# Kernel optimization log

Measured on AMD Instinct MI355X. Metric: run time of the kernel, lower is better.

Reference implementation:

```python
import jax, jax.numpy as jnp
import numpy as np

ALPHA = 1e-4
BETA = 1.0
MAX_STD = 1000.0
MIN_STD = 1.0
B = 8192            # number of ragged segments (batch)
NUM_CLASSES = 2
P = 1_000_000       # size of penalized parameter vector


def setup_inputs() -> dict:
    key = jax.random.key(0)
    k1, k2, k3, k4 = jax.random.split(key, 4)
    # ragged lengths: alternate 1024 / 3072, exact total T = B * 2048
    lengths = np.where(np.arange(B) % 2 == 0, 1024, 3072).astype(np.int32)
    T = int(lengths.sum())  # 16_777_216
    seg = np.repeat(np.arange(B, dtype=np.int32), lengths)
    starts = np.concatenate([[0], np.cumsum(lengths)[:-1]])
    local = np.arange(T, dtype=np.int64) - np.repeat(starts, lengths)
    # get_x: positions (1..len)/len within each segment
    xpos = ((local + 1).astype(np.float64) / np.repeat(lengths, lengths)).astype(np.float32)
    return {
        "logits": jax.random.normal(k1, (B, NUM_CLASSES), jnp.float32),
        "labels": jax.random.randint(k2, (B,), 0, 2, jnp.int32),
        "attention_weights": jax.random.uniform(k3, (T,), jnp.float32),
        "params": jax.random.normal(k4, (P,), jnp.float32),
        "xpos": jnp.asarray(xpos),
        "segment_ids": jnp.asarray(seg),
        "lengths": jnp.asarray(lengths),
    }


def reference(logits, labels, attention_weights, params, xpos, segment_ids, lengths):
    nseg = logits.shape[0]
    lens_f = lengths.astype(jnp.float32)

    # CrossEntropyLoss (mean reduction)
    logp = jax.nn.log_softmax(logits, axis=-1)
    nll = -jnp.mean(jnp.take_along_axis(logp, labels[:, None].astype(jnp.int32), axis=1))

    # --- no-grad block: per-segment mean and ideal-gaussian target r ---
    w = jax.lax.stop_gradient(attention_weights)
    sum_w = jax.ops.segment_sum(w, segment_ids, num_segments=nseg)          # [B]
    mean = jax.ops.segment_sum(xpos * w, segment_ids, num_segments=nseg) / sum_w
    ideal_std = jnp.where(labels == 1, MIN_STD, MAX_STD) / lens_f           # [B]
    mu_t = mean[segment_ids]                                                # [T]
    std_t = ideal_std[segment_ids]                                          # [T]
    z = (xpos - mu_t) / std_t
    r_hat = jnp.exp(-0.5 * z * z) / (std_t * jnp.sqrt(2.0 * jnp.pi))        # normal pdf
    r_sum = jax.ops.segment_sum(r_hat, segment_ids, num_segments=nseg)
    r = r_hat / (r_sum[segment_ids] + 1e-6)
    r = jax.lax.stop_gradient(r)

    # L1 penalty on params
    penalty = ALPHA / 2 * jnp.abs(params).sum()

    # per-segment mean of squared diff, then mean over segments
    diff2 = (attention_weights - r) ** 2
    per_seg = jax.ops.segment_sum(diff2, segment_ids, num_segments=nseg) / lens_f
    awp = BETA / 2 * per_seg.mean()

    loss = nll + penalty + awp
    return jnp.stack([loss, nll])
```

## Files before the change

kernel.cpp:

```cpp
#include <hip/hip_runtime.h>


#define TPB 256
#define PARAM_BLOCKS 256

__device__ __forceinline__ void blockReduce3(float& a, float& b, float& c,
                                             float* sm) {
  #pragma unroll
  for (int off = 32; off > 0; off >>= 1) {
    a += __shfl_xor(a, off, 64);
    b += __shfl_xor(b, off, 64);
    c += __shfl_xor(c, off, 64);
  }
  const int lane = threadIdx.x & 63, wid = threadIdx.x >> 6;
  if (lane == 0) { sm[wid] = a; sm[4 + wid] = b; sm[8 + wid] = c; }
  __syncthreads();
  a = sm[0] + sm[1] + sm[2] + sm[3];
  b = sm[4] + sm[5] + sm[6] + sm[7];
  c = sm[8] + sm[9] + sm[10] + sm[11];
}

__device__ __forceinline__ float blockReduceSum(float v, float* sm) {
  #pragma unroll
  for (int off = 32; off > 0; off >>= 1) v += __shfl_xor(v, off, 64);
  const int lane = threadIdx.x & 63, wid = threadIdx.x >> 6;
  if (lane == 0) sm[wid] = v;
  __syncthreads();
  return sm[0] + sm[1] + sm[2] + sm[3];
}

__global__ __launch_bounds__(TPB)
void scan_kernel(const int* __restrict__ lengths, int nseg,
                 int* __restrict__ starts) {
  __shared__ int wsum[4];
  const int t = threadIdx.x;
  const int per = (nseg + TPB - 1) / TPB;
  const int base = t * per;
  int local = 0;
  for (int j = 0; j < per; j++) {
    int idx = base + j;
    if (idx < nseg) local += lengths[idx];
  }
  const int lane = t & 63, wid = t >> 6;
  int incl = local;
  #pragma unroll
  for (int off = 1; off < 64; off <<= 1) {
    int n = __shfl_up(incl, off, 64);
    if (lane >= off) incl += n;
  }
  if (lane == 63) wsum[wid] = incl;
  __syncthreads();
  int wbase = 0;
  for (int i = 0; i < wid; i++) wbase += wsum[i];
  int run = wbase + incl - local;
  for (int j = 0; j < per; j++) {
    int idx = base + j;
    if (idx < nseg) { starts[idx] = run; run += lengths[idx]; }
  }
}

template <int NC>
__device__ __forceinline__ float seg_body(const float4* __restrict__ w4,
                                          int start4, int len, int lab,
                                          float* sm) {
  const float inv_len = 1.0f / (float)len;
  float4 wv[NC];
  float aw = 0.0f, axw = 0.0f, aww = 0.0f;
  #pragma unroll
  for (int k = 0; k < NC; k++) {
    const int vi = (k << 8) + threadIdx.x;
    wv[k] = w4[start4 + vi];
    const int i0 = vi << 2;
    aw += wv[k].x + wv[k].y + wv[k].z + wv[k].w;
    axw = fmaf((float)(i0 + 1) * inv_len, wv[k].x, axw);
    axw = fmaf((float)(i0 + 2) * inv_len, wv[k].y, axw);
    axw = fmaf((float)(i0 + 3) * inv_len, wv[k].z, axw);
    axw = fmaf((float)(i0 + 4) * inv_len, wv[k].w, axw);
    aww = fmaf(wv[k].x, wv[k].x, aww);
    aww = fmaf(wv[k].y, wv[k].y, aww);
    aww = fmaf(wv[k].z, wv[k].z, aww);
    aww = fmaf(wv[k].w, wv[k].w, aww);
  }
  blockReduce3(aw, axw, aww, sm);
  const float mean = axw / aw;
  const float invstd = (float)len * (lab == 1 ? 1.0f : 0.001f);
  const float rn = 0.39894228040143267f * invstd;
  const float c1 = inv_len * invstd;
  const float m2 = mean * invstd;
  float ar = 0.0f, awr = 0.0f, arr = 0.0f;
  #pragma unroll
  for (int k = 0; k < NC; k++) {
    const int i0 = (((k << 8) + threadIdx.x)) << 2;
    float z0 = fmaf((float)(i0 + 1), c1, -m2);
    float z1 = fmaf((float)(i0 + 2), c1, -m2);
    float z2 = fmaf((float)(i0 + 3), c1, -m2);
    float z3 = fmaf((float)(i0 + 4), c1, -m2);
    float r0 = __expf(-0.5f * z0 * z0) * rn;
    float r1 = __expf(-0.5f * z1 * z1) * rn;
    float r2 = __expf(-0.5f * z2 * z2) * rn;
    float r3 = __expf(-0.5f * z3 * z3) * rn;
    ar += r0 + r1 + r2 + r3;
    awr = fmaf(wv[k].x, r0, awr); awr = fmaf(wv[k].y, r1, awr);
    awr = fmaf(wv[k].z, r2, awr); awr = fmaf(wv[k].w, r3, awr);
    arr = fmaf(r0, r0, arr); arr = fmaf(r1, r1, arr);
    arr = fmaf(r2, r2, arr); arr = fmaf(r3, r3, arr);
  }
  blockReduce3(ar, awr, arr, sm + 12);
  const float rinv = 1.0f / (ar + 1e-6f);
  const float dsum = aww - 2.0f * rinv * awr + rinv * rinv * arr;
  return dsum * inv_len;
}

__device__ float seg_generic(const float* __restrict__ w, int start, int len,
                             int lab, float* sm) {
  const float inv_len = 1.0f / (float)len;
  float aw = 0.0f, axw = 0.0f, aww = 0.0f;
  for (int i = threadIdx.x; i < len; i += TPB) {
    float wv = w[start + i];
    aw += wv;
    axw = fmaf((float)(i + 1) * inv_len, wv, axw);
    aww = fmaf(wv, wv, aww);
  }
  blockReduce3(aw, axw, aww, sm);
  const float mean = axw / aw;
  const float invstd = (float)len * (lab == 1 ? 1.0f : 0.001f);
  const float rn = 0.39894228040143267f * invstd;
  float ar = 0.0f, awr = 0.0f, arr = 0.0f;
  for (int i = threadIdx.x; i < len; i += TPB) {
    float z = ((float)(i + 1) * inv_len - mean) * invstd;
    float rh = __expf(-0.5f * z * z) * rn;
    ar += rh;
    awr = fmaf(w[start + i], rh, awr);
    arr = fmaf(rh, rh, arr);
  }
  blockReduce3(ar, awr, arr, sm + 12);
  const float rinv = 1.0f / (ar + 1e-6f);
  const float dsum = aww - 2.0f * rinv * awr + rinv * rinv * arr;
  return dsum * inv_len;
}

__global__ __launch_bounds__(TPB)
void main_kernel(const float* __restrict__ attw, const float* __restrict__ params,
                 const float* __restrict__ logits, const int* __restrict__ labels,
                 const int* __restrict__ lengths, const int* __restrict__ starts,
                 int nseg, int P, float* __restrict__ partial) {
  __shared__ float sm[24];
  const int b = blockIdx.x;
  if (b < nseg) {
    const int len = lengths[b];
    const int start = starts[b];
    const int lab = labels[b];
    float r;
    if (len == 1024 && (start & 3) == 0)
      r = seg_body<1>((const float4*)attw, start >> 2, len, lab, sm);
    else if (len == 3072 && (start & 3) == 0)
      r = seg_body<3>((const float4*)attw, start >> 2, len, lab, sm);
    else
      r = seg_generic(attw, start, len, lab, sm);
    if (threadIdx.x == 0) partial[b] = r;
  } else if (b < nseg + PARAM_BLOCKS) {
    const int pb = b - nseg;
    const int P4 = P >> 2;
    const float4* p4 = (const float4*)params;
    float a = 0.0f;
    for (int i = pb * TPB + threadIdx.x; i < P4; i += PARAM_BLOCKS * TPB) {
      float4 v = p4[i];
      a += fabsf(v.x) + fabsf(v.y) + fabsf(v.z) + fabsf(v.w);
    }
    if (pb == 0 && threadIdx.x == 0)
      for (int i = P4 << 2; i < P; i++) a += fabsf(params[i]);
    float tot = blockReduceSum(a, sm);
    if (threadIdx.x == 0) partial[nseg + pb] = tot;
  } else {
    float acc = 0.0f;
    for (int s = threadIdx.x; s < nseg; s += TPB) {
      float l0 = logits[2 * s], l1 = logits[2 * s + 1];
      int lab = labels[s];
      float m = fmaxf(l0, l1);
      float lse = m + logf(expf(l0 - m) + expf(l1 - m));
      acc += (lab ? l1 : l0) - lse;
    }
    float tot = blockReduceSum(acc, sm);
    if (threadIdx.x == 0) partial[nseg + PARAM_BLOCKS] = tot;
  }
}

__global__ __launch_bounds__(TPB)
void finalize_kernel(const float* __restrict__ partial, int nseg,
                     float* __restrict__ out) {
  __shared__ float sm[8];
  float a_awp = 0.0f, a_abs = 0.0f;
  for (int i = threadIdx.x; i < nseg; i += TPB) a_awp += partial[i];
  for (int i = threadIdx.x; i < PARAM_BLOCKS; i += TPB) a_abs += partial[nseg + i];
  #pragma unroll
  for (int off = 32; off > 0; off >>= 1) {
    a_awp += __shfl_xor(a_awp, off, 64);
    a_abs += __shfl_xor(a_abs, off, 64);
  }
  const int lane = threadIdx.x & 63, wid = threadIdx.x >> 6;
  if (lane == 0) { sm[wid] = a_awp; sm[4 + wid] = a_abs; }
  __syncthreads();
  if (threadIdx.x == 0) {
    float s_awp = sm[0] + sm[1] + sm[2] + sm[3];
    float s_abs = sm[4] + sm[5] + sm[6] + sm[7];
    const float nll = -partial[nseg + PARAM_BLOCKS] / (float)nseg;
    const float penalty = 0.5f * 1e-4f * s_abs;
    const float awp = 0.5f * (s_awp / (float)nseg);
    out[0] = nll + penalty + awp;
    out[1] = nll;
  }
}

extern "C" void kernel_launch(void* const* d_in, const int* in_sizes, int n_in,
                              void* d_out, int out_size, void* d_ws, size_t ws_size,
                              hipStream_t stream) {
  const float* logits  = (const float*)d_in[0];
  const int*   labels  = (const int*)d_in[1];
  const float* attw    = (const float*)d_in[2];
  const float* params  = (const float*)d_in[3];
  const int*   lengths = (const int*)d_in[6];
  const int nseg = in_sizes[1];
  const int P    = in_sizes[3];

  int* starts = (int*)d_ws;
  size_t poff = ((size_t)nseg * sizeof(int) + 255) & ~(size_t)255;
  float* partial = (float*)((char*)d_ws + poff);
  float* out = (float*)d_out;

  scan_kernel<<<1, TPB, 0, stream>>>(lengths, nseg, starts);
  main_kernel<<<nseg + PARAM_BLOCKS + 1, TPB, 0, stream>>>(
      attw, params, logits, labels, lengths, starts, nseg, P, partial);
  finalize_kernel<<<1, TPB, 0, stream>>>(partial, nseg, out);
}
```

Baseline: 210.5 us.

## Drop scan kernel; compute segment starts per block via redundant prefix sum

Removes the single-block scan launch. Each segment block now computes its own start offset by summing all preceding lengths with a block reduction. The logits and param blocks are moved to the front of the grid so they are scheduled first, and the cross-entropy now uses fast-math intrinsics. This saves one kernel launch and its serial dependency, but adds O(B^2) redundant length reads in total: up to 8192 reads per block, mostly served from cache.

```diff
diff --git a/kernel.cpp b/kernel.cpp
--- a/kernel.cpp
+++ b/kernel.cpp
@@ -27,36 +27,6 @@
   if (lane == 0) sm[wid] = v;
   __syncthreads();
   return sm[0] + sm[1] + sm[2] + sm[3];
-}
-
-__global__ __launch_bounds__(TPB)
-void scan_kernel(const int* __restrict__ lengths, int nseg,
-                 int* __restrict__ starts) {
-  __shared__ int wsum[4];
-  const int t = threadIdx.x;
-  const int per = (nseg + TPB - 1) / TPB;
-  const int base = t * per;
-  int local = 0;
-  for (int j = 0; j < per; j++) {
-    int idx = base + j;
-    if (idx < nseg) local += lengths[idx];
-  }
-  const int lane = t & 63, wid = t >> 6;
-  int incl = local;
-  #pragma unroll
-  for (int off = 1; off < 64; off <<= 1) {
-    int n = __shfl_up(incl, off, 64);
-    if (lane >= off) incl += n;
-  }
-  if (lane == 63) wsum[wid] = incl;
-  __syncthreads();
-  int wbase = 0;
-  for (int i = 0; i < wid; i++) wbase += wsum[i];
-  int run = wbase + incl - local;
-  for (int j = 0; j < per; j++) {
-    int idx = base + j;
-    if (idx < nseg) { starts[idx] = run; run += lengths[idx]; }
-  }
 }
 
 template <int NC>
@@ -142,24 +112,24 @@
 __global__ __launch_bounds__(TPB)
 void main_kernel(const float* __restrict__ attw, const float* __restrict__ params,
                  const float* __restrict__ logits, const int* __restrict__ labels,
-                 const int* __restrict__ lengths, const int* __restrict__ starts,
-                 int nseg, int P, float* __restrict__ partial) {
+                 const int* __restrict__ lengths, int nseg, int P,
+                 float* __restrict__ partial) {
   __shared__ float sm[24];
+  __shared__ int smi[4];
   const int b = blockIdx.x;
-  if (b < nseg) {
-    const int len = lengths[b];
-    const int start = starts[b];
-    const int lab = labels[b];
-    float r;
-    if (len == 1024 && (start & 3) == 0)
-      r = seg_body<1>((const float4*)attw, start >> 2, len, lab, sm);
-    else if (len == 3072 && (start & 3) == 0)
-      r = seg_body<3>((const float4*)attw, start >> 2, len, lab, sm);
-    else
-      r = seg_generic(attw, start, len, lab, sm);
-    if (threadIdx.x == 0) partial[b] = r;
-  } else if (b < nseg + PARAM_BLOCKS) {
-    const int pb = b - nseg;
+  if (b == 0) {
+    float acc = 0.0f;
+    for (int s = threadIdx.x; s < nseg; s += TPB) {
+      float l0 = logits[2 * s], l1 = logits[2 * s + 1];
+      int lab = labels[s];
+      float m = fmaxf(l0, l1);
+      float lse = m + __logf(__expf(l0 - m) + __expf(l1 - m));
+      acc += (lab ? l1 : l0) - lse;
+    }
+    float tot = blockReduceSum(acc, sm);
+    if (threadIdx.x == 0) partial[nseg + PARAM_BLOCKS] = tot;
+  } else if (b <= PARAM_BLOCKS) {
+    const int pb = b - 1;
     const int P4 = P >> 2;
     const float4* p4 = (const float4*)params;
     float a = 0.0f;
@@ -172,16 +142,26 @@
     float tot = blockReduceSum(a, sm);
     if (threadIdx.x == 0) partial[nseg + pb] = tot;
   } else {
-    float acc = 0.0f;
-    for (int s = threadIdx.x; s < nseg; s += TPB) {
-      float l0 = logits[2 * s], l1 = logits[2 * s + 1];
-      int lab = labels[s];
-      float m = fmaxf(l0, l1);
-      float lse = m + logf(expf(l0 - m) + expf(l1 - m));
-      acc += (lab ? l1 : l0) - lse;
-    }
-    float tot = blockReduceSum(acc, sm);
-    if (threadIdx.x == 0) partial[nseg + PARAM_BLOCKS] = tot;
+    const int seg = b - 1 - PARAM_BLOCKS;
+    if (seg >= nseg) return;
+    int acc = 0;
+    for (int i = threadIdx.x; i < seg; i += TPB) acc += lengths[i];
+    #pragma unroll
+    for (int off = 32; off > 0; off >>= 1) acc += __shfl_xor(acc, off, 64);
+    const int lane = threadIdx.x & 63, wid = threadIdx.x >> 6;
+    if (lane == 0) smi[wid] = acc;
+    __syncthreads();
+    const int start = smi[0] + smi[1] + smi[2] + smi[3];
+    const int len = lengths[seg];
+    const int lab = labels[seg];
+    float r;
+    if (len == 1024 && (start & 3) == 0)
+      r = seg_body<1>((const float4*)attw, start >> 2, len, lab, sm);
+    else if (len == 3072 && (start & 3) == 0)
+      r = seg_body<3>((const float4*)attw, start >> 2, len, lab, sm);
+    else
+      r = seg_generic(attw, start, len, lab, sm);
+    if (threadIdx.x == 0) partial[seg] = r;
   }
 }
 
@@ -222,13 +202,10 @@
   const int nseg = in_sizes[1];
   const int P    = in_sizes[3];
 
-  int* starts = (int*)d_ws;
-  size_t poff = ((size_t)nseg * sizeof(int) + 255) & ~(size_t)255;
-  float* partial = (float*)((char*)d_ws + poff);
+  float* partial = (float*)d_ws;
   float* out = (float*)d_out;
 
-  scan_kernel<<<1, TPB, 0, stream>>>(lengths, nseg, starts);
-  main_kernel<<<nseg + PARAM_BLOCKS + 1, TPB, 0, stream>>>(
-      attw, params, logits, labels, lengths, starts, nseg, P, partial);
+  main_kernel<<<1 + PARAM_BLOCKS + nseg, TPB, 0, stream>>>(
+      attw, params, logits, labels, lengths, nseg, P, partial);
   finalize_kernel<<<1, TPB, 0, stream>>>(partial, nseg, out);
 }
```

Result: faster. 188.3 us (-10.5%).
